# Kernel optimization log

Hardware: AMD Instinct MI355X
Metric: run time of the kernel (lower is better)

The kernel has to match this reference:

```python
import jax, jax.numpy as jnp
import numpy as np
import math

DIM = 1024
MAX_SEQ_LEN = 8192

def setup_inputs() -> dict:
    key = jax.random.key(0)
    k1, k2, k3, k4 = jax.random.split(key, 4)
    x = jax.random.normal(k1, (4, 4096, DIM), dtype=jnp.float32)
    base_phases = jax.random.normal(k2, (MAX_SEQ_LEN, DIM), dtype=jnp.float32) * math.pi
    # nn.Linear(dim, dim): weight [out, in], bias [out]
    bound = 1.0 / math.sqrt(DIM)
    W = jax.random.uniform(k3, (DIM, DIM), dtype=jnp.float32, minval=-bound, maxval=bound)
    b = jax.random.uniform(k4, (DIM,), dtype=jnp.float32, minval=-bound, maxval=bound)
    return {"x": x, "base_phases": base_phases, "W": W, "b": b}

def reference(x, base_phases, W, b):
    B, L, D = x.shape
    phases = base_phases[:L][None, :, :]          # [1, L, D]
    value = jnp.einsum('bld,ed->ble', x, W) + b   # Linear: x @ W.T + b
    cos_p = jnp.cos(phases)
    sin_p = jnp.sin(phases)
    mem_real = jnp.cumsum(value * cos_p, axis=1)
    mem_imag = jnp.cumsum(value * sin_p, axis=1)
    retrieved = mem_real * cos_p + mem_imag * sin_p
    positions = jnp.arange(1, L + 1, dtype=jnp.float32)
    norm = jnp.sqrt(positions)[None, :, None]     # [1, L, 1]
    return retrieved / norm
```

## Files before the change

### kernel.cpp

```cpp
#include <hip/hip_runtime.h>
#include <hip/hip_bf16.h>

#define DIM 1024
#define SEQ 4096
#define NB 4
#define MROWS (NB * SEQ)
#define NC 64
#define CL (SEQ / NC)

#define BM 256
#define BN 256
#define BK 32
#define NTK 32
#define SLOTB 49152
#define GEMM_LDS (3 * SLOTB)

typedef __attribute__((ext_vector_type(8))) short bf16x8;
typedef __attribute__((ext_vector_type(4))) float f32x4;

static __device__ __forceinline__ unsigned short f2bf(float f) {
    union { float f; unsigned u; } v; v.f = f;
    unsigned r = v.u + 0x7FFF + ((v.u >> 16) & 1);
    return (unsigned short)(r >> 16);
}

static __device__ __forceinline__ float bf2f(unsigned short h) {
    union { unsigned u; float f; } v; v.u = ((unsigned)h) << 16;
    return v.f;
}

static __device__ __forceinline__ unsigned cvtpk(float a, float b) {
    unsigned r;
    asm("v_cvt_pk_bf16_f32 %0, %1, %2" : "=v"(r) : "v"(a), "v"(b));
    return r;
}

static __device__ __forceinline__ void gload_lds16(const void* g, void* l) {
    __builtin_amdgcn_global_load_lds((const __attribute__((address_space(1))) void*)g,
                                     (__attribute__((address_space(3))) void*)l, 16, 0, 0);
}

template<int CTRL>
static __device__ __forceinline__ float dppadd(float x) {
    int y = __builtin_amdgcn_update_dpp(0, __float_as_int(x), CTRL, 0xf, 0xf, true);
    return x + __int_as_float(y);
}
static __device__ __forceinline__ float rowreduce16(float x) {
    x = dppadd<0xB1>(x);
    x = dppadd<0x4E>(x);
    x = dppadd<0x141>(x);
    x = dppadd<0x140>(x);
    return x;
}

__global__ void convertW_kernel(const float* __restrict__ W, unsigned short* __restrict__ wb) {
    int t = blockIdx.x * 256 + threadIdx.x;
    float4 v = ((const float4*)W)[t];
    ushort4 o;
    o.x = f2bf(v.x); o.y = f2bf(v.y); o.z = f2bf(v.z); o.w = f2bf(v.w);
    ((ushort4*)wb)[t] = o;
}

static __device__ __forceinline__ void stage_Af32(const float* __restrict__ srcBase, char* smem,
                                                  int slot, int kt, int w, int lane) {
#pragma unroll
    for (int j = 0; j < 4; ++j) {
        const float* g = srcBase + (size_t)j * 8 * DIM + kt * BK;
        char* l = smem + (size_t)slot * SLOTB + (w * 4 + j) * 1024 + lane * 16;
        gload_lds16(g, l);
    }
}

static __device__ __forceinline__ void stage_B16(const unsigned short* __restrict__ srcBase, char* smem,
                                                 int slot, int kt, int w, int lane) {
#pragma unroll
    for (int r = 0; r < 2; ++r) {
        const unsigned short* g = srcBase + (size_t)r * 128 * DIM + kt * BK;
        char* l = smem + (size_t)slot * SLOTB + 32768 + (r * 128 + w * 16) * 64 + lane * 16;
        gload_lds16(g, l);
    }
}

__global__ __launch_bounds__(512, 2) void gemm_kernel(const float* __restrict__ X,
                                                      const unsigned short* __restrict__ Bm,
                                                      const float* __restrict__ bias,
                                                      const float* __restrict__ ph,
                                                      unsigned short* __restrict__ V,
                                                      float* __restrict__ pr,
                                                      float* __restrict__ pi) {
    extern __shared__ char smem[];
    const int tid  = threadIdx.x;
    const int lane = tid & 63;
    const int w    = tid >> 6;
    const int wr   = (w >> 2) * 128;
    const int wc   = (w & 3) * 64;
    const int rl   = lane & 15;
    const int rh   = lane >> 4;
    const int m0   = blockIdx.x * BM;
    const int n0   = blockIdx.y * BN;

    const float* srcA = X + (size_t)(m0 + w * 32 + (lane >> 3)) * DIM + ((lane & 7) ^ (lane >> 3)) * 4;
    const unsigned short* srcB = Bm + (size_t)(n0 + w * 16 + (lane >> 2)) * DIM
                               + (((lane & 3) ^ ((lane >> 3) & 3)) * 8);

    const int swzB = (rh ^ ((rl >> 1) & 3)) * 16;
    const int aoff0 = (wr + rl) * 128 + (((rh * 2 + 0) ^ (rl & 7)) * 16);
    const int aoff1 = (wr + rl) * 128 + (((rh * 2 + 1) ^ (rl & 7)) * 16);

    f32x4 acc[8][4];
#pragma unroll
    for (int m = 0; m < 8; ++m)
#pragma unroll
        for (int n = 0; n < 4; ++n)
            acc[m][n] = (f32x4){0.f, 0.f, 0.f, 0.f};

    f32x4 bv4[4];
#pragma unroll
    for (int nf = 0; nf < 4; ++nf)
        bv4[nf] = *(const f32x4*)(bias + n0 + wc + nf * 16 + rh * 4);

    stage_Af32(srcA, smem, 0, 0, w, lane);
    stage_B16 (srcB, smem, 0, 0, w, lane);
    stage_Af32(srcA, smem, 1, 1, w, lane);
    stage_B16 (srcB, smem, 1, 1, w, lane);

#pragma unroll 1
    for (int t = 0; t < NTK; ++t) {
        asm volatile("s_waitcnt vmcnt(6)" ::: "memory");
        __builtin_amdgcn_s_barrier();
        const int sc = t % 3;
        const int ss = (t + 2) % 3;
        const int kn = (t + 2) & (NTK - 1);
        const char* sb = smem + (size_t)sc * SLOTB;

        bf16x8 bfr[4];
#pragma unroll
        for (int nf = 0; nf < 4; ++nf)
            bfr[nf] = *(const bf16x8*)(sb + 32768 + (wc + nf * 16 + rl) * 64 + swzB);

        bf16x8 af[4];
#pragma unroll
        for (int mf = 0; mf < 4; ++mf) {
            f32x4 q0 = *(const f32x4*)(sb + mf * 2048 + aoff0);
            f32x4 q1 = *(const f32x4*)(sb + mf * 2048 + aoff1);
            union { unsigned u[4]; bf16x8 v; } cv;
            cv.u[0] = cvtpk(q0[0], q0[1]); cv.u[1] = cvtpk(q0[2], q0[3]);
            cv.u[2] = cvtpk(q1[0], q1[1]); cv.u[3] = cvtpk(q1[2], q1[3]);
            af[mf] = cv.v;
        }
        stage_Af32(srcA, smem, ss, kn, w, lane);
        __builtin_amdgcn_s_setprio(1);
#pragma unroll
        for (int mf = 0; mf < 4; ++mf)
#pragma unroll
            for (int nf = 0; nf < 4; ++nf)
                acc[mf][nf] = __builtin_amdgcn_mfma_f32_16x16x32_bf16(bfr[nf], af[mf], acc[mf][nf], 0, 0, 0);
        __builtin_amdgcn_s_setprio(0);

#pragma unroll
        for (int mf = 0; mf < 4; ++mf) {
            f32x4 q0 = *(const f32x4*)(sb + (mf + 4) * 2048 + aoff0);
            f32x4 q1 = *(const f32x4*)(sb + (mf + 4) * 2048 + aoff1);
            union { unsigned u[4]; bf16x8 v; } cv;
            cv.u[0] = cvtpk(q0[0], q0[1]); cv.u[1] = cvtpk(q0[2], q0[3]);
            cv.u[2] = cvtpk(q1[0], q1[1]); cv.u[3] = cvtpk(q1[2], q1[3]);
            af[mf] = cv.v;
        }
        stage_B16(srcB, smem, ss, kn, w, lane);
        __builtin_amdgcn_s_setprio(1);
#pragma unroll
        for (int mf = 0; mf < 4; ++mf)
#pragma unroll
            for (int nf = 0; nf < 4; ++nf)
                acc[mf + 4][nf] = __builtin_amdgcn_mfma_f32_16x16x32_bf16(bfr[nf], af[mf], acc[mf + 4][nf], 0, 0, 0);
        __builtin_amdgcn_s_setprio(0);
    }

    const int bb = m0 >> 12;
    const int lb = (m0 & (SEQ - 1)) + wr;
    float csr[2][4][4], csi[2][4][4];
#pragma unroll
    for (int h = 0; h < 2; ++h)
#pragma unroll
        for (int nf = 0; nf < 4; ++nf)
#pragma unroll
            for (int j = 0; j < 4; ++j) { csr[h][nf][j] = 0.f; csi[h][nf][j] = 0.f; }

#pragma unroll
    for (int mf = 0; mf < 8; ++mf) {
        const int l    = lb + mf * 16 + rl;
        const int grow = m0 + wr + mf * 16 + rl;
        const int half = mf >> 2;
#pragma unroll
        for (int nf = 0; nf < 4; ++nf) {
            const int gcol0 = n0 + wc + nf * 16 + rh * 4;
            f32x4 pp = *(const f32x4*)(ph + (size_t)l * DIM + gcol0);
            unsigned short os[4];
#pragma unroll
            for (int j = 0; j < 4; ++j) {
                float v = acc[mf][nf][j] + bv4[nf][j];
                float s, cn;
                __sincosf(pp[j], &s, &cn);
                csr[half][nf][j] += v * cn;
                csi[half][nf][j] += v * s;
                os[j] = f2bf(v);
            }
            ushort4 o; o.x = os[0]; o.y = os[1]; o.z = os[2]; o.w = os[3];
            *(ushort4*)(V + (size_t)grow * DIM + gcol0) = o;
        }
    }
#pragma unroll
    for (int h = 0; h < 2; ++h)
#pragma unroll
        for (int nf = 0; nf < 4; ++nf)
#pragma unroll
            for (int j = 0; j < 4; ++j) {
                csr[h][nf][j] = rowreduce16(csr[h][nf][j]);
                csi[h][nf][j] = rowreduce16(csi[h][nf][j]);
            }
    if (rl == 0) {
#pragma unroll
        for (int h = 0; h < 2; ++h) {
            const int c = (lb + h * 64) >> 6;
            const size_t base = ((size_t)bb * NC + c) * DIM;
#pragma unroll
            for (int nf = 0; nf < 4; ++nf) {
                const int gcol0 = n0 + wc + nf * 16 + rh * 4;
                *(float4*)(pr + base + gcol0) =
                    (float4){csr[h][nf][0], csr[h][nf][1], csr[h][nf][2], csr[h][nf][3]};
                *(float4*)(pi + base + gcol0) =
                    (float4){csi[h][nf][0], csi[h][nf][1], csi[h][nf][2], csi[h][nf][3]};
            }
        }
    }
}

__global__ void passB_kernel(float* __restrict__ pr, float* __restrict__ pi) {
    int t = blockIdx.x * 256 + threadIdx.x;
    int bb = t >> 10;
    int e  = t & 1023;
    float r = 0.f, im = 0.f;
    for (int c = 0; c < NC; ++c) {
        size_t idx = ((size_t)bb * NC + c) * DIM + e;
        float tr = pr[idx], ti = pi[idx];
        pr[idx] = r; pi[idx] = im;
        r += tr; im += ti;
    }
}

__global__ void passC_kernel(const unsigned short* __restrict__ val, const float* __restrict__ ph,
                             const float* __restrict__ pr, const float* __restrict__ pi,
                             float* __restrict__ out) {
    int t  = blockIdx.x * 256 + threadIdx.x;
    int c  = blockIdx.y;
    int bb = blockIdx.z;
    size_t base = ((size_t)bb * SEQ + (size_t)c * CL) * (DIM / 2) + t;
    const ushort2* v = (const ushort2*)val + base;
    const float2*  p = (const float2*)ph + (size_t)c * CL * (DIM / 2) + t;
    float2* o = (float2*)out + base;
    size_t pidx = ((size_t)bb * NC + c) * DIM + 2 * t;
    float ar0 = pr[pidx], ar1 = pr[pidx + 1];
    float ai0 = pi[pidx], ai1 = pi[pidx + 1];
    const int l0 = c * CL;
    for (int l = 0; l < CL; ++l) {
        ushort2 vv = v[(size_t)l * (DIM / 2)];
        float2  pp = p[(size_t)l * (DIM / 2)];
        float v0 = bf2f(vv.x), v1 = bf2f(vv.y);
        float s0, c0, s1, c1;
        __sincosf(pp.x, &s0, &c0);
        __sincosf(pp.y, &s1, &c1);
        ar0 += v0 * c0; ai0 += v0 * s0;
        ar1 += v1 * c1; ai1 += v1 * s1;
        float rn = rsqrtf((float)(l0 + l + 1));
        float2 ov;
        ov.x = (ar0 * c0 + ai0 * s0) * rn;
        ov.y = (ar1 * c1 + ai1 * s1) * rn;
        o[(size_t)l * (DIM / 2)] = ov;
    }
}

extern "C" void kernel_launch(void* const* d_in, const int* in_sizes, int n_in,
                              void* d_out, int out_size, void* d_ws, size_t ws_size,
                              hipStream_t stream) {
    const float* x  = (const float*)d_in[0];
    const float* ph = (const float*)d_in[1];
    const float* W  = (const float*)d_in[2];
    const float* b  = (const float*)d_in[3];
    float* out = (float*)d_out;

    unsigned short* vb = (unsigned short*)d_ws;
    unsigned short* wb = vb + (size_t)MROWS * DIM;
    float* pr = (float*)(wb + (size_t)DIM * DIM);
    float* pi = pr + (size_t)NB * NC * DIM;

    (void)hipFuncSetAttribute((const void*)gemm_kernel,
                              hipFuncAttributeMaxDynamicSharedMemorySize, GEMM_LDS);

    convertW_kernel<<<DIM * DIM / 4 / 256, 256, 0, stream>>>(W, wb);
    {
        dim3 grid(MROWS / BM, DIM / BN);
        gemm_kernel<<<grid, 512, GEMM_LDS, stream>>>(x, wb, b, ph, vb, pr, pi);
    }
    passB_kernel<<<16, 256, 0, stream>>>(pr, pi);
    {
        dim3 grid(DIM / 512, NC, NB);
        passC_kernel<<<grid, 256, 0, stream>>>(vb, ph, pr, pi, out);
    }
}
```

Measured before the change: 84.34 us.

## Remap GEMM row tile to span four batches of one sequence chunk

```diff
diff --git a/kernel.cpp b/kernel.cpp
--- a/kernel.cpp
+++ b/kernel.cpp
@@ -92,14 +92,17 @@
     const int tid  = threadIdx.x;
     const int lane = tid & 63;
     const int w    = tid >> 6;
-    const int wr   = (w >> 2) * 128;
+    const int wm   = w >> 2;
+    const int wr   = wm * 128;
     const int wc   = (w & 3) * 64;
     const int rl   = lane & 15;
     const int rh   = lane >> 4;
-    const int m0   = blockIdx.x * BM;
+    const int cx   = blockIdx.x;
+    const int c0   = cx * 64;
     const int n0   = blockIdx.y * BN;
 
-    const float* srcA = X + (size_t)(m0 + w * 32 + (lane >> 3)) * DIM + ((lane & 7) ^ (lane >> 3)) * 4;
+    const float* srcA = X + (size_t)((w >> 1) * SEQ + c0 + (w & 1) * 32 + (lane >> 3)) * DIM
+                      + ((lane & 7) ^ (lane >> 3)) * 4;
     const unsigned short* srcB = Bm + (size_t)(n0 + w * 16 + (lane >> 2)) * DIM
                                + (((lane & 3) ^ ((lane >> 3) & 3)) * 8);
 
@@ -176,8 +179,14 @@
         __builtin_amdgcn_s_setprio(0);
     }
 
-    const int bb = m0 >> 12;
-    const int lb = (m0 & (SEQ - 1)) + wr;
+#pragma unroll
+    for (int mf = 0; mf < 8; ++mf)
+#pragma unroll
+        for (int nf = 0; nf < 4; ++nf)
+#pragma unroll
+            for (int j = 0; j < 4; ++j)
+                acc[mf][nf][j] += bv4[nf][j];
+
     float csr[2][4][4], csi[2][4][4];
 #pragma unroll
     for (int h = 0; h < 2; ++h)
@@ -187,28 +196,33 @@
             for (int j = 0; j < 4; ++j) { csr[h][nf][j] = 0.f; csi[h][nf][j] = 0.f; }
 
 #pragma unroll
-    for (int mf = 0; mf < 8; ++mf) {
-        const int l    = lb + mf * 16 + rl;
-        const int grow = m0 + wr + mf * 16 + rl;
-        const int half = mf >> 2;
+    for (int mq = 0; mq < 4; ++mq) {
+        const int l = c0 + mq * 16 + rl;
+        const size_t grow0 = (size_t)(wm * 2) * SEQ + l;
+        const size_t grow1 = grow0 + SEQ;
 #pragma unroll
         for (int nf = 0; nf < 4; ++nf) {
             const int gcol0 = n0 + wc + nf * 16 + rh * 4;
             f32x4 pp = *(const f32x4*)(ph + (size_t)l * DIM + gcol0);
-            unsigned short os[4];
+            ushort4 o0, o1;
+            unsigned short* p0 = (unsigned short*)&o0;
+            unsigned short* p1 = (unsigned short*)&o1;
 #pragma unroll
             for (int j = 0; j < 4; ++j) {
-                float v = acc[mf][nf][j] + bv4[nf][j];
                 float s, cn;
                 __sincosf(pp[j], &s, &cn);
-                csr[half][nf][j] += v * cn;
-                csi[half][nf][j] += v * s;
-                os[j] = f2bf(v);
+                float v0 = acc[mq][nf][j];
+                float v1 = acc[mq + 4][nf][j];
+                csr[0][nf][j] += v0 * cn; csi[0][nf][j] += v0 * s;
+                csr[1][nf][j] += v1 * cn; csi[1][nf][j] += v1 * s;
+                p0[j] = f2bf(v0);
+                p1[j] = f2bf(v1);
             }
-            ushort4 o; o.x = os[0]; o.y = os[1]; o.z = os[2]; o.w = os[3];
-            *(ushort4*)(V + (size_t)grow * DIM + gcol0) = o;
+            *(ushort4*)(V + grow0 * DIM + gcol0) = o0;
+            *(ushort4*)(V + grow1 * DIM + gcol0) = o1;
         }
     }
+
 #pragma unroll
     for (int h = 0; h < 2; ++h)
 #pragma unroll
@@ -221,8 +235,8 @@
     if (rl == 0) {
 #pragma unroll
         for (int h = 0; h < 2; ++h) {
-            const int c = (lb + h * 64) >> 6;
-            const size_t base = ((size_t)bb * NC + c) * DIM;
+            const int b = wm * 2 + h;
+            const size_t base = ((size_t)b * NC + cx) * DIM;
 #pragma unroll
             for (int nf = 0; nf < 4; ++nf) {
                 const int gcol0 = n0 + wc + nf * 16 + rh * 4;
@@ -298,7 +312,7 @@
 
     convertW_kernel<<<DIM * DIM / 4 / 256, 256, 0, stream>>>(W, wb);
     {
-        dim3 grid(MROWS / BM, DIM / BN);
+        dim3 grid(NC, DIM / BN);
         gemm_kernel<<<grid, 512, GEMM_LDS, stream>>>(x, wb, b, ph, vb, pr, pi);
     }
     passB_kernel<<<16, 256, 0, stream>>>(pr, pi);
```

Result: slower. 92.06 us (+9.1%).
